# Kernel tuning notes

Hardware: AMD Instinct MI355X
Metric: run time of the kernel (lower is better)

The kernel has to match this reference:

```python
import jax, jax.numpy as jnp
import numpy as np

D_MODEL = 512
HEADS = 8

def setup_inputs() -> dict:
    key = jax.random.key(0)
    ks = jax.random.split(key, 11)
    B, S, D = 2, 4096, D_MODEL
    s = 1.0 / np.sqrt(D)
    inp = {
        'q': jax.random.normal(ks[0], (B, S, D), jnp.float32),
        'k': jax.random.normal(ks[1], (B, S, D), jnp.float32),
        'v': jax.random.normal(ks[2], (B, S, D), jnp.float32),
        'Wq': jax.random.normal(ks[3], (D, D), jnp.float32) * s,
        'bq': jnp.zeros((D,), jnp.float32),
        'Wk': jax.random.normal(ks[4], (D, D), jnp.float32) * s,
        'bk': jnp.zeros((D,), jnp.float32),
        'Wv': jax.random.normal(ks[5], (D, D), jnp.float32) * s,
        'bv': jnp.zeros((D,), jnp.float32),
        'Wo': jax.random.normal(ks[6], (D, D), jnp.float32) * s,
        'bo': jnp.zeros((D,), jnp.float32),
    }
    return inp

def _split_heads(x, h):
    B, S, D = x.shape
    return x.reshape(B, S, h, D // h).transpose(0, 2, 1, 3)  # [B,H,S,Dh]

def reference(q, k, v, Wq, bq, Wk, bk, Wv, bv, Wo, bo):
    # torch Linear: y = x @ W.T + b
    qh = _split_heads(q @ Wq.T + bq, HEADS)
    kh = _split_heads(k @ Wk.T + bk, HEADS)
    vh = _split_heads(v @ Wv.T + bv, HEADS)
    d_tensor = qh.shape[-1]
    scale = 1.0 / jnp.sqrt(jnp.asarray(d_tensor, qh.dtype))
    score = jnp.einsum('bhqd,bhkd->bhqk', qh, kh) * scale  # [B,H,S,S]
    attn = jax.nn.softmax(score, axis=-1)
    out = jnp.einsum('bhqk,bhkd->bhqd', attn, vh)
    B, H, S, Dh = out.shape
    out = out.transpose(0, 2, 1, 3).reshape(B, S, H * Dh)
    return out @ Wo.T + bo
```

## Files before the change

### kernel.cpp

```cpp
#include <hip/hip_runtime.h>

typedef short bf16x8 __attribute__((ext_vector_type(8)));
typedef float f32x2 __attribute__((ext_vector_type(2)));
typedef float f32x4 __attribute__((ext_vector_type(4)));
typedef float f32x16 __attribute__((ext_vector_type(16)));
typedef unsigned short ushort_t;
typedef unsigned short us8 __attribute__((ext_vector_type(8)));
typedef unsigned short us4 __attribute__((ext_vector_type(4)));
typedef unsigned int u32x4 __attribute__((ext_vector_type(4)));
typedef unsigned int uint2v __attribute__((ext_vector_type(2)));

#define MFMA16(a, b, c) __builtin_amdgcn_mfma_f32_16x16x32_bf16((a), (b), (c), 0, 0, 0)
#define MFMA32(a, b, c) __builtin_amdgcn_mfma_f32_32x32x16_bf16((a), (b), (c), 0, 0, 0)

template <int N> struct ic { static constexpr int value = N; };

static __device__ __forceinline__ ushort_t f2bf(float f) {
    unsigned int u = __builtin_bit_cast(unsigned int, f);
    u += 0x7FFFu + ((u >> 16) & 1u);
    return (ushort_t)(u >> 16);
}

static __device__ __forceinline__ unsigned cvtpk(float lo, float hi) {
    unsigned r;
    asm("v_cvt_pk_bf16_f32 %0, %1, %2" : "=v"(r) : "v"(lo), "v"(hi));
    return r;
}

static __device__ __forceinline__ void gload16(const void* g, void* l) {
    __builtin_amdgcn_global_load_lds(
        (const __attribute__((address_space(1))) unsigned int*)g,
        (__attribute__((address_space(3))) unsigned int*)l,
        16, 0, 0);
}

__global__ __launch_bounds__(256) void cvt_w(const float* __restrict__ W0,
                                             const float* __restrict__ W1,
                                             const float* __restrict__ W2,
                                             const float* __restrict__ W3,
                                             ushort_t* __restrict__ dst) {
    const float* src = (blockIdx.y == 0) ? W0 : (blockIdx.y == 1) ? W1
                     : (blockIdx.y == 2) ? W2 : W3;
    const int i = (blockIdx.x * 256 + threadIdx.x) * 8;
    float4 f0 = *(const float4*)(src + i);
    float4 f1 = *(const float4*)(src + i + 4);
    unsigned tw[4] = {cvtpk(f0.x, f0.y), cvtpk(f0.z, f0.w),
                      cvtpk(f1.x, f1.y), cvtpk(f1.z, f1.w)};
    *(u32x4*)(dst + (size_t)blockIdx.y * 262144 + i) = *(u32x4*)tw;
}

__global__ __launch_bounds__(256) void gemm_qkv(const float* __restrict__ qi,
                                                const float* __restrict__ ki,
                                                const float* __restrict__ vi,
                                                const ushort_t* __restrict__ Wball,
                                                const float* __restrict__ bq,
                                                const float* __restrict__ bk,
                                                const float* __restrict__ bv,
                                                ushort_t* __restrict__ Qh,
                                                ushort_t* __restrict__ Kh,
                                                ushort_t* __restrict__ Vt,
                                                float Cs) {
    constexpr int K = 512;
    __shared__ ushort_t As[64][72];
    __shared__ ushort_t Bs[64][72];

    const int which = blockIdx.y;
    const float*    Ap   = (which == 0) ? qi : (which == 1) ? ki : vi;
    const ushort_t* Wb   = Wball + (size_t)which * 262144;
    const float*    bias = (which == 0) ? bq : (which == 1) ? bk : bv;
    ushort_t*       outp = (which == 0) ? Qh : (which == 1) ? Kh : Vt;

    int bid = blockIdx.x;
    bid = (bid & 7) * 128 + (bid >> 3);
    const int bm = bid >> 3;
    const int bn = bid & 7;
    const int m0 = bm * 64, n0 = bn * 64;
    const int t    = threadIdx.x;
    const int lane = t & 63;
    const int wv   = t >> 6;
    const int wm   = wv >> 1, wn = wv & 1;
    const int lrow = t >> 2;
    const int lcol = (t & 3) * 16;

    const int l15 = lane & 15;
    const int l16 = lane >> 4;

    f32x4 acc[2][2] = {};

    const float*    apf = Ap + (size_t)(m0 + lrow) * K + lcol;
    const ushort_t* bpb = Wb + (size_t)(n0 + lrow) * K + lcol;

    us8 br0, br1;
    f32x4 af[4];

    af[0] = *(const f32x4*)apf;       af[1] = *(const f32x4*)(apf + 4);
    af[2] = *(const f32x4*)(apf + 8); af[3] = *(const f32x4*)(apf + 12);
    br0 = *(const us8*)bpb; br1 = *(const us8*)(bpb + 8);

#pragma unroll 1
    for (int kt = 0; kt < K / 64; ++kt) {
        __syncthreads();
        {
            unsigned tw[8];
#pragma unroll
            for (int i = 0; i < 4; ++i) {
                tw[2 * i]     = cvtpk(af[i][0], af[i][1]);
                tw[2 * i + 1] = cvtpk(af[i][2], af[i][3]);
            }
            *(u32x4*)&As[lrow][lcol]     = *(u32x4*)tw;
            *(u32x4*)&As[lrow][lcol + 8] = *(u32x4*)(tw + 4);
        }
        *(us8*)&Bs[lrow][lcol]     = br0;
        *(us8*)&Bs[lrow][lcol + 8] = br1;
        __syncthreads();

        if (kt < K / 64 - 1) {
            const int off = (kt + 1) * 64;
            const float* s = apf + off;
            af[0] = *(const f32x4*)s;       af[1] = *(const f32x4*)(s + 4);
            af[2] = *(const f32x4*)(s + 8); af[3] = *(const f32x4*)(s + 12);
            br0 = *(const us8*)(bpb + off); br1 = *(const us8*)(bpb + off + 8);
        }

#pragma unroll
        for (int kk = 0; kk < 2; ++kk) {
            bf16x8 a0 = *(const bf16x8*)&As[wm * 32 + l15][kk * 32 + l16 * 8];
            bf16x8 a1 = *(const bf16x8*)&As[wm * 32 + 16 + l15][kk * 32 + l16 * 8];
            bf16x8 b0 = *(const bf16x8*)&Bs[wn * 32 + l15][kk * 32 + l16 * 8];
            bf16x8 b1 = *(const bf16x8*)&Bs[wn * 32 + 16 + l15][kk * 32 + l16 * 8];
            acc[0][0] = MFMA16(a0, b0, acc[0][0]);
            acc[0][1] = MFMA16(a0, b1, acc[0][1]);
            acc[1][0] = MFMA16(a1, b0, acc[1][0]);
            acc[1][1] = MFMA16(a1, b1, acc[1][1]);
        }
    }

#pragma unroll
    for (int i = 0; i < 2; ++i)
#pragma unroll
        for (int j = 0; j < 2; ++j) {
            const int n  = n0 + wn * 32 + j * 16 + l15;
            const float bv_ = bias[n];
            const int h = n >> 6, d = n & 63;
            if (which == 2) {
                const int mbase = m0 + wm * 32 + i * 16 + l16 * 4;
                const int b = mbase >> 12, key = mbase & 4095;
                const int keyr = key & 63;
                const int ks = keyr >> 4, hc = (keyr >> 3) & 1, e0 = keyr & 7;
                const int db = d >> 5, dr = d & 31;
                ushort_t tmp[4];
#pragma unroll
                for (int v = 0; v < 4; ++v) tmp[v] = f2bf(acc[i][j][v] + bv_);
                *(us4*)(outp + (size_t)(b * 8 + h) * 262144 +
                        (size_t)(key >> 6) * 4096 +
                        db * 2048 + ks * 512 + (hc * 32 + dr) * 8 + e0) = *(us4*)tmp;
            } else if (which == 1) {
                const int jd = d >> 4, hc = (d >> 3) & 1, e = d & 7;
#pragma unroll
                for (int v = 0; v < 4; ++v) {
                    const int m = m0 + wm * 32 + i * 16 + l16 * 4 + v;
                    const int b = m >> 12, s = m & 4095;
                    const int r = s & 63, kb2 = r >> 5, kr = r & 31;
                    outp[(size_t)(b * 8 + h) * 262144 + (size_t)(s >> 6) * 4096 +
                         kb2 * 2048 + jd * 512 + (hc * 32 + kr) * 8 + e] =
                        f2bf(acc[i][j][v] + bv_);
                }
            } else {
#pragma unroll
                for (int v = 0; v < 4; ++v) {
                    const int m = m0 + wm * 32 + i * 16 + l16 * 4 + v;
                    const int b = m >> 12, s = m & 4095;
                    outp[(((size_t)(b * 8 + h)) * 4096 + s) * 64 + d] =
                        f2bf((acc[i][j][v] + bv_) * Cs);
                }
            }
        }
}

__global__ __launch_bounds__(256) void gemm_out(const ushort_t* __restrict__ Ap,
                                                const ushort_t* __restrict__ Wb,
                                                const float* __restrict__ bias,
                                                float* __restrict__ outp) {
    constexpr int K = 512;
    __shared__ ushort_t As[64][72];
    __shared__ ushort_t Bs[64][72];

    int bid = blockIdx.x;
    bid = (bid & 7) * 128 + (bid >> 3);
    const int bm = bid >> 3;
    const int bn = bid & 7;
    const int m0 = bm * 64, n0 = bn * 64;
    const int t    = threadIdx.x;
    const int lane = t & 63;
    const int wv   = t >> 6;
    const int wm   = wv >> 1, wn = wv & 1;
    const int lrow = t >> 2;
    const int lcol = (t & 3) * 16;

    const int l15 = lane & 15;
    const int l16 = lane >> 4;

    f32x4 acc[2][2] = {};

    const ushort_t* apb = Ap + (size_t)(m0 + lrow) * K + lcol;
    const ushort_t* bpb = Wb + (size_t)(n0 + lrow) * K + lcol;

    us8 ar0, ar1, br0, br1;
    ar0 = *(const us8*)apb; ar1 = *(const us8*)(apb + 8);
    br0 = *(const us8*)bpb; br1 = *(const us8*)(bpb + 8);

#pragma unroll 1
    for (int kt = 0; kt < K / 64; ++kt) {
        __syncthreads();
        *(us8*)&As[lrow][lcol]     = ar0;
        *(us8*)&As[lrow][lcol + 8] = ar1;
        *(us8*)&Bs[lrow][lcol]     = br0;
        *(us8*)&Bs[lrow][lcol + 8] = br1;
        __syncthreads();

        if (kt < K / 64 - 1) {
            const int off = (kt + 1) * 64;
            ar0 = *(const us8*)(apb + off); ar1 = *(const us8*)(apb + off + 8);
            br0 = *(const us8*)(bpb + off); br1 = *(const us8*)(bpb + off + 8);
        }

#pragma unroll
        for (int kk = 0; kk < 2; ++kk) {
            bf16x8 a0 = *(const bf16x8*)&As[wm * 32 + l15][kk * 32 + l16 * 8];
            bf16x8 a1 = *(const bf16x8*)&As[wm * 32 + 16 + l15][kk * 32 + l16 * 8];
            bf16x8 b0 = *(const bf16x8*)&Bs[wn * 32 + l15][kk * 32 + l16 * 8];
            bf16x8 b1 = *(const bf16x8*)&Bs[wn * 32 + 16 + l15][kk * 32 + l16 * 8];
            acc[0][0] = MFMA16(a0, b0, acc[0][0]);
            acc[0][1] = MFMA16(a0, b1, acc[0][1]);
            acc[1][0] = MFMA16(a1, b0, acc[1][0]);
            acc[1][1] = MFMA16(a1, b1, acc[1][1]);
        }
    }

#pragma unroll
    for (int i = 0; i < 2; ++i)
#pragma unroll
        for (int j = 0; j < 2; ++j) {
            const int n  = n0 + wn * 32 + j * 16 + l15;
            const float bv_ = bias[n];
#pragma unroll
            for (int v = 0; v < 4; ++v) {
                const int m = m0 + wm * 32 + i * 16 + l16 * 4 + v;
                outp[(size_t)m * 512 + n] = acc[i][j][v] + bv_;
            }
        }
}

__global__ __launch_bounds__(256) void attn_fwd(const ushort_t* __restrict__ Qh,
                                                const ushort_t* __restrict__ Kg,
                                                const ushort_t* __restrict__ Vg,
                                                ushort_t* __restrict__ Out) {
    constexpr int S  = 4096;
    __shared__ __attribute__((aligned(16))) char LDS[40960];

    const int id   = blockIdx.x;
    const int xcd  = id & 7;
    const int slot = id >> 3;
    const int qt   = slot & 31;
    const int bh   = xcd * 2 + (slot >> 5);
    const int b    = bh >> 3, h = bh & 7;

    const int t    = threadIdx.x;
    const int lane = t & 63;
    const int wv   = t >> 6;
    const int l31  = lane & 31;
    const int hl   = lane >> 5;

    const int qw = qt * 128 + wv * 32;

    bf16x8 qf[4];
    {
        const ushort_t* qp = Qh + ((size_t)bh * S + qw + l31) * 64 + hl * 8;
#pragma unroll
        for (int ds = 0; ds < 4; ++ds) qf[ds] = *(const bf16x8*)(qp + ds * 16);
    }

    const f32x16 fzero = {};
    f32x16 accO[2] = {};
    float ll = 0.f;

    const char* lbase = LDS + lane * 16;
    const int wvb = wv * 1024;
    const ushort_t* kg = Kg + (size_t)bh * 262144 + wv * 512 + lane * 8;
    const ushort_t* vg = Vg + (size_t)bh * 262144 + wv * 512 + lane * 8;

    auto issueK = [&](int kt, int kslotB) {
        const ushort_t* p = kg + (size_t)kt * 4096;
        gload16(p,        LDS + kslotB + wvb);
        gload16(p + 2048, LDS + kslotB + 4096 + wvb);
    };
    auto issueV = [&](int kt, int vslotB) {
        const ushort_t* p = vg + (size_t)kt * 4096;
        gload16(p,        LDS + vslotB + wvb);
        gload16(p + 2048, LDS + vslotB + 4096 + wvb);
    };

    auto QK = [&](auto kc, f32x16& s0, f32x16& s1) {
        constexpr int KB = decltype(kc)::value;
        __builtin_amdgcn_s_setprio(1);
        {
            bf16x8 kf = *(const bf16x8*)(lbase + KB);
            s0 = MFMA32(kf, qf[0], fzero);
        }
#pragma unroll
        for (int ds = 1; ds < 4; ++ds) {
            bf16x8 kf = *(const bf16x8*)(lbase + KB + ds * 1024);
            s0 = MFMA32(kf, qf[ds], s0);
        }
        {
            bf16x8 kf = *(const bf16x8*)(lbase + KB + 4096);
            s1 = MFMA32(kf, qf[0], fzero);
        }
#pragma unroll
        for (int ds = 1; ds < 4; ++ds) {
            bf16x8 kf = *(const bf16x8*)(lbase + KB + 4096 + ds * 1024);
            s1 = MFMA32(kf, qf[ds], s1);
        }
        __builtin_amdgcn_s_setprio(0);
    };

    auto SOFTPV = [&](f32x16& sc0, f32x16& sc1, int vbase) {
#pragma unroll
        for (int i = 0; i < 16; ++i) {
            sc0[i] = __builtin_amdgcn_exp2f(sc0[i]);
            sc1[i] = __builtin_amdgcn_exp2f(sc1[i]);
        }
        {
#define PAIR(v, i) __builtin_shufflevector((v), (v), 2 * (i), 2 * (i) + 1)
            f32x2 pa  = (PAIR(sc0, 0) + PAIR(sc0, 1)) + (PAIR(sc0, 2) + PAIR(sc0, 3));
            f32x2 pbt = (PAIR(sc0, 4) + PAIR(sc0, 5)) + (PAIR(sc0, 6) + PAIR(sc0, 7));
            f32x2 pc  = (PAIR(sc1, 0) + PAIR(sc1, 1)) + (PAIR(sc1, 2) + PAIR(sc1, 3));
            f32x2 pd  = (PAIR(sc1, 4) + PAIR(sc1, 5)) + (PAIR(sc1, 6) + PAIR(sc1, 7));
            f32x2 s2  = (pa + pbt) + (pc + pd);
            ll += s2.x + s2.y;
#undef PAIR
        }
        bf16x8 pb[4];
#pragma unroll
        for (int ks = 0; ks < 4; ++ks) {
            const int R0 = (ks & 1) * 8;
            float e0, e1, e2, e3, e4, e5, e6, e7;
            if (ks < 2) {
                e0 = sc0[R0+0]; e1 = sc0[R0+1]; e2 = sc0[R0+2]; e3 = sc0[R0+3];
                e4 = sc0[R0+4]; e5 = sc0[R0+5]; e6 = sc0[R0+6]; e7 = sc0[R0+7];
            } else {
                e0 = sc1[R0+0]; e1 = sc1[R0+1]; e2 = sc1[R0+2]; e3 = sc1[R0+3];
                e4 = sc1[R0+4]; e5 = sc1[R0+5]; e6 = sc1[R0+6]; e7 = sc1[R0+7];
            }
            unsigned w0 = cvtpk(e0, e1);
            unsigned w1 = cvtpk(e2, e3);
            unsigned w2 = cvtpk(e4, e5);
            unsigned w3 = cvtpk(e6, e7);
            uint2v s02 = __builtin_amdgcn_permlane32_swap(w0, w2, false, false);
            uint2v s13 = __builtin_amdgcn_permlane32_swap(w1, w3, false, false);
            u32x4 w = {s02.x, s13.x, s02.y, s13.y};
            pb[ks] = __builtin_bit_cast(bf16x8, w);
        }
        const char* vb = LDS + vbase + lane * 16;
        __builtin_amdgcn_s_setprio(1);
#pragma unroll
        for (int ks = 0; ks < 4; ++ks) {
            {
                bf16x8 vf = *(const bf16x8*)(vb + ks * 1024);
                accO[0] = MFMA32(vf, pb[ks], accO[0]);
            }
            {
                bf16x8 vf = *(const bf16x8*)(vb + 4096 + ks * 1024);
                accO[1] = MFMA32(vf, pb[ks], accO[1]);
            }
        }
        __builtin_amdgcn_s_setprio(0);
    };

    int v0b = 16384, v1b = 24576, v2b = 32768;

    issueK(0, 0);
    issueK(1, 8192);
    issueV(0, v0b);
    issueV(1, v1b);
    __syncthreads();

    f32x16 sA0, sA1, sB0, sB1;
    QK(ic<0>{}, sA0, sA1);

#pragma unroll 1
    for (int tp = 0; tp < 31; ++tp) {
        const int te = 2 * tp;
        __syncthreads();
        issueK(te + 2, 0);
        issueV(te + 2, v2b);
        QK(ic<8192>{}, sB0, sB1);
        SOFTPV(sA0, sA1, v0b);
        { int tmp = v0b; v0b = v1b; v1b = v2b; v2b = tmp; }
        __syncthreads();
        issueK(te + 3, 8192);
        issueV(te + 3, v2b);
        QK(ic<0>{}, sA0, sA1);
        SOFTPV(sB0, sB1, v0b);
        { int tmp = v0b; v0b = v1b; v1b = v2b; v2b = tmp; }
    }

    __syncthreads();
    QK(ic<8192>{}, sB0, sB1);
    SOFTPV(sA0, sA1, v0b);
    { int tmp = v0b; v0b = v1b; v1b = v2b; v2b = tmp; }

    SOFTPV(sB0, sB1, v0b);

    const float lt  = ll + __shfl_xor(ll, 32);
    const float inv = 1.0f / lt;
    ushort_t* orow = Out + ((size_t)b * S + qw + l31) * 512 + h * 64;
#pragma unroll
    for (int db = 0; db < 2; ++db)
#pragma unroll
        for (int q4 = 0; q4 < 4; ++q4) {
            unsigned w0 = cvtpk(accO[db][q4 * 4 + 0] * inv, accO[db][q4 * 4 + 1] * inv);
            unsigned w1 = cvtpk(accO[db][q4 * 4 + 2] * inv, accO[db][q4 * 4 + 3] * inv);
            unsigned tmp[2] = {w0, w1};
            *(us4*)(orow + db * 32 + q4 * 8 + hl * 4) = *(const us4*)tmp;
        }
}

extern "C" void kernel_launch(void* const* d_in, const int* in_sizes, int n_in,
                              void* d_out, int out_size, void* d_ws, size_t ws_size,
                              hipStream_t stream) {
    const float* q  = (const float*)d_in[0];
    const float* k  = (const float*)d_in[1];
    const float* v  = (const float*)d_in[2];
    const float* Wq = (const float*)d_in[3];
    const float* bq = (const float*)d_in[4];
    const float* bk = (const float*)d_in[6];
    const float* bv = (const float*)d_in[8];
    const float* bo = (const float*)d_in[10];

    char* w = (char*)d_ws;
    const size_t SZ = (size_t)2 * 8 * 4096 * 64 * 2;

    ushort_t* Qh  = (ushort_t*)(w);
    ushort_t* Kh  = (ushort_t*)(w + SZ);
    ushort_t* Vtr = (ushort_t*)(w + 2 * SZ);
    ushort_t* AO  = (ushort_t*)(w + 3 * SZ);
    ushort_t* Wb  = (ushort_t*)(w + 4 * SZ);

    cvt_w<<<dim3(128, 4), 256, 0, stream>>>(Wq, (const float*)d_in[5],
                                            (const float*)d_in[7], (const float*)d_in[9], Wb);

    const float Cs = 0.125f * 1.44269504f;
    gemm_qkv<<<dim3(1024, 3), 256, 0, stream>>>(q, k, v, Wb, bq, bk, bv, Qh, Kh, Vtr, Cs);

    attn_fwd<<<512, 256, 0, stream>>>(Qh, Kh, Vtr, AO);

    gemm_out<<<1024, 256, 0, stream>>>(AO, Wb + 3 * 262144, bo, (float*)d_out);
}
```

Before: 136.8 us.

## Pre-tile weights and attention output into MFMA fragment order, load via global_load_lds

The weight conversion kernel now writes bf16 weights pre-permuted into per-tile MFMA fragment order, and the attention kernel writes its output in the same tiled layout. Both GEMMs can then fetch tiles with direct global-to-LDS 16-byte loads into double-buffered LDS, with no register staging or padded shared arrays. This is meant to cut register round-trips and LDS store instructions and to overlap the next tile's fetch with the MFMA work. It couples three kernels to one custom layout, and gemm_out now uses one barrier per iteration, which relies on the async load completing before that barrier.

```diff
diff --git a/kernel.cpp b/kernel.cpp
--- a/kernel.cpp
+++ b/kernel.cpp
@@ -42,11 +42,19 @@
     const float* src = (blockIdx.y == 0) ? W0 : (blockIdx.y == 1) ? W1
                      : (blockIdx.y == 2) ? W2 : W3;
     const int i = (blockIdx.x * 256 + threadIdx.x) * 8;
+    const int n = i >> 9, k = i & 511;
     float4 f0 = *(const float4*)(src + i);
     float4 f1 = *(const float4*)(src + i + 4);
     unsigned tw[4] = {cvtpk(f0.x, f0.y), cvtpk(f0.z, f0.w),
                       cvtpk(f1.x, f1.y), cvtpk(f1.z, f1.w)};
-    *(u32x4*)(dst + (size_t)blockIdx.y * 262144 + i) = *(u32x4*)tw;
+    const int bn = n >> 6, r = n & 63;
+    const int wn = r >> 5, j = (r >> 4) & 1, l15 = r & 15;
+    const int kt = k >> 6, c = k & 63;
+    const int kk = c >> 5, l16 = (c >> 3) & 3;
+    const size_t off = (size_t)blockIdx.y * 262144 +
+        (size_t)((bn * 8 + kt) * 4096 + (wn * 4 + j * 2 + kk) * 512 +
+                 (l16 * 16 + l15) * 8);
+    *(u32x4*)(dst + off) = *(u32x4*)tw;
 }
 
 __global__ __launch_bounds__(256) void gemm_qkv(const float* __restrict__ qi,
@@ -62,7 +70,7 @@
                                                 float Cs) {
     constexpr int K = 512;
     __shared__ ushort_t As[64][72];
-    __shared__ ushort_t Bs[64][72];
+    __shared__ __attribute__((aligned(16))) char Bimg[16384];
 
     const int which = blockIdx.y;
     const float*    Ap   = (which == 0) ? qi : (which == 1) ? ki : vi;
@@ -88,17 +96,22 @@
     f32x4 acc[2][2] = {};
 
     const float*    apf = Ap + (size_t)(m0 + lrow) * K + lcol;
-    const ushort_t* bpb = Wb + (size_t)(n0 + lrow) * K + lcol;
-
-    us8 br0, br1;
+    const ushort_t* wgp = Wb + (size_t)bn * 8 * 4096 + wv * 1024 + lane * 8;
+
+    auto issueB = [&](int kt, int cur) {
+        const ushort_t* p = wgp + (size_t)kt * 4096;
+        gload16(p,       Bimg + cur * 8192 + wv * 2048);
+        gload16(p + 512, Bimg + cur * 8192 + wv * 2048 + 1024);
+    };
+
     f32x4 af[4];
-
     af[0] = *(const f32x4*)apf;       af[1] = *(const f32x4*)(apf + 4);
     af[2] = *(const f32x4*)(apf + 8); af[3] = *(const f32x4*)(apf + 12);
-    br0 = *(const us8*)bpb; br1 = *(const us8*)(bpb + 8);
+    issueB(0, 0);
 
 #pragma unroll 1
     for (int kt = 0; kt < K / 64; ++kt) {
+        const int cur = kt & 1;
         __syncthreads();
         {
             unsigned tw[8];
@@ -110,24 +123,22 @@
             *(u32x4*)&As[lrow][lcol]     = *(u32x4*)tw;
             *(u32x4*)&As[lrow][lcol + 8] = *(u32x4*)(tw + 4);
         }
-        *(us8*)&Bs[lrow][lcol]     = br0;
-        *(us8*)&Bs[lrow][lcol + 8] = br1;
         __syncthreads();
 
         if (kt < K / 64 - 1) {
-            const int off = (kt + 1) * 64;
-            const float* s = apf + off;
+            issueB(kt + 1, cur ^ 1);
+            const float* s = apf + (kt + 1) * 64;
             af[0] = *(const f32x4*)s;       af[1] = *(const f32x4*)(s + 4);
             af[2] = *(const f32x4*)(s + 8); af[3] = *(const f32x4*)(s + 12);
-            br0 = *(const us8*)(bpb + off); br1 = *(const us8*)(bpb + off + 8);
-        }
-
+        }
+
+        const char* lbB = Bimg + cur * 8192 + wn * 4096 + lane * 16;
 #pragma unroll
         for (int kk = 0; kk < 2; ++kk) {
             bf16x8 a0 = *(const bf16x8*)&As[wm * 32 + l15][kk * 32 + l16 * 8];
             bf16x8 a1 = *(const bf16x8*)&As[wm * 32 + 16 + l15][kk * 32 + l16 * 8];
-            bf16x8 b0 = *(const bf16x8*)&Bs[wn * 32 + l15][kk * 32 + l16 * 8];
-            bf16x8 b1 = *(const bf16x8*)&Bs[wn * 32 + 16 + l15][kk * 32 + l16 * 8];
+            bf16x8 b0 = *(const bf16x8*)(lbB + kk * 1024);
+            bf16x8 b1 = *(const bf16x8*)(lbB + 2048 + kk * 1024);
             acc[0][0] = MFMA16(a0, b0, acc[0][0]);
             acc[0][1] = MFMA16(a0, b1, acc[0][1]);
             acc[1][0] = MFMA16(a1, b0, acc[1][0]);
@@ -177,13 +188,11 @@
         }
 }
 
-__global__ __launch_bounds__(256) void gemm_out(const ushort_t* __restrict__ Ap,
-                                                const ushort_t* __restrict__ Wb,
+__global__ __launch_bounds__(256) void gemm_out(const ushort_t* __restrict__ AOc,
+                                                const ushort_t* __restrict__ Wo,
                                                 const float* __restrict__ bias,
                                                 float* __restrict__ outp) {
-    constexpr int K = 512;
-    __shared__ ushort_t As[64][72];
-    __shared__ ushort_t Bs[64][72];
+    __shared__ __attribute__((aligned(16))) char Img[32768];
 
     int bid = blockIdx.x;
     bid = (bid & 7) * 128 + (bid >> 3);
@@ -194,47 +203,45 @@
     const int lane = t & 63;
     const int wv   = t >> 6;
     const int wm   = wv >> 1, wn = wv & 1;
-    const int lrow = t >> 2;
-    const int lcol = (t & 3) * 16;
-
-    const int l15 = lane & 15;
-    const int l16 = lane >> 4;
+    const int l15  = lane & 15;
+    const int l16  = lane >> 4;
 
     f32x4 acc[2][2] = {};
 
-    const ushort_t* apb = Ap + (size_t)(m0 + lrow) * K + lcol;
-    const ushort_t* bpb = Wb + (size_t)(n0 + lrow) * K + lcol;
-
-    us8 ar0, ar1, br0, br1;
-    ar0 = *(const us8*)apb; ar1 = *(const us8*)(apb + 8);
-    br0 = *(const us8*)bpb; br1 = *(const us8*)(bpb + 8);
+    const ushort_t* agp = AOc + (size_t)bm * 8 * 4096 + wv * 1024 + lane * 8;
+    const ushort_t* bgp = Wo  + (size_t)bn * 8 * 4096 + wv * 1024 + lane * 8;
+
+    auto issue = [&](int kt, int cur) {
+        const ushort_t* pa = agp + (size_t)kt * 4096;
+        gload16(pa,       Img + cur * 8192 + wv * 2048);
+        gload16(pa + 512, Img + cur * 8192 + wv * 2048 + 1024);
+        const ushort_t* pb = bgp + (size_t)kt * 4096;
+        gload16(pb,       Img + 16384 + cur * 8192 + wv * 2048);
+        gload16(pb + 512, Img + 16384 + cur * 8192 + wv * 2048 + 1024);
+    };
+
+    issue(0, 0);
+    __syncthreads();
 
 #pragma unroll 1
-    for (int kt = 0; kt < K / 64; ++kt) {
-        __syncthreads();
-        *(us8*)&As[lrow][lcol]     = ar0;
-        *(us8*)&As[lrow][lcol + 8] = ar1;
-        *(us8*)&Bs[lrow][lcol]     = br0;
-        *(us8*)&Bs[lrow][lcol + 8] = br1;
-        __syncthreads();
-
-        if (kt < K / 64 - 1) {
-            const int off = (kt + 1) * 64;
-            ar0 = *(const us8*)(apb + off); ar1 = *(const us8*)(apb + off + 8);
-            br0 = *(const us8*)(bpb + off); br1 = *(const us8*)(bpb + off + 8);
-        }
-
+    for (int kt = 0; kt < 8; ++kt) {
+        const int cur = kt & 1;
+        if (kt < 7) issue(kt + 1, cur ^ 1);
+
+        const char* lbA = Img + cur * 8192 + wm * 4096 + lane * 16;
+        const char* lbB = Img + 16384 + cur * 8192 + wn * 4096 + lane * 16;
 #pragma unroll
         for (int kk = 0; kk < 2; ++kk) {
-            bf16x8 a0 = *(const bf16x8*)&As[wm * 32 + l15][kk * 32 + l16 * 8];
-            bf16x8 a1 = *(const bf16x8*)&As[wm * 32 + 16 + l15][kk * 32 + l16 * 8];
-            bf16x8 b0 = *(const bf16x8*)&Bs[wn * 32 + l15][kk * 32 + l16 * 8];
-            bf16x8 b1 = *(const bf16x8*)&Bs[wn * 32 + 16 + l15][kk * 32 + l16 * 8];
+            bf16x8 a0 = *(const bf16x8*)(lbA + kk * 1024);
+            bf16x8 a1 = *(const bf16x8*)(lbA + 2048 + kk * 1024);
+            bf16x8 b0 = *(const bf16x8*)(lbB + kk * 1024);
+            bf16x8 b1 = *(const bf16x8*)(lbB + 2048 + kk * 1024);
             acc[0][0] = MFMA16(a0, b0, acc[0][0]);
             acc[0][1] = MFMA16(a0, b1, acc[0][1]);
             acc[1][0] = MFMA16(a1, b0, acc[1][0]);
             acc[1][1] = MFMA16(a1, b1, acc[1][1]);
         }
+        __syncthreads();
     }
 
 #pragma unroll
@@ -409,12 +416,16 @@
     QK(ic<8192>{}, sB0, sB1);
     SOFTPV(sA0, sA1, v0b);
     { int tmp = v0b; v0b = v1b; v1b = v2b; v2b = tmp; }
-
     SOFTPV(sB0, sB1, v0b);
 
     const float lt  = ll + __shfl_xor(ll, 32);
     const float inv = 1.0f / lt;
-    ushort_t* orow = Out + ((size_t)b * S + qw + l31) * 512 + h * 64;
+    const int mrow = qw + l31;
+    const int bmA  = b * 64 + (mrow >> 6);
+    const int rr   = mrow & 63;
+    const int wmr  = rr >> 5, i2r = (rr >> 4) & 1, l15r = rr & 15;
+    ushort_t* obase = Out + ((size_t)bmA * 8 + h) * 4096 +
+                      (size_t)(wmr * 4 + i2r * 2) * 512 + l15r * 8 + hl * 4;
 #pragma unroll
     for (int db = 0; db < 2; ++db)
 #pragma unroll
@@ -422,7 +433,7 @@
             unsigned w0 = cvtpk(accO[db][q4 * 4 + 0] * inv, accO[db][q4 * 4 + 1] * inv);
             unsigned w1 = cvtpk(accO[db][q4 * 4 + 2] * inv, accO[db][q4 * 4 + 3] * inv);
             unsigned tmp[2] = {w0, w1};
-            *(us4*)(orow + db * 32 + q4 * 8 + hl * 4) = *(const us4*)tmp;
+            *(us4*)(obase + db * 512 + q4 * 128) = *(const us4*)tmp;
         }
 }
 
```

New measurement: 134.3 us (median of 2 runs). About the same (-1.8%).
